# Optimization experiments

Measured on AMD Instinct MI355X. Metric: run time of the kernel, lower is better.

Reference implementation:

```python
import jax, jax.numpy as jnp
import numpy as np

EPS = 1e-5
B, T, C, E, K, D, BN = 8, 2048, 3, 256, 15, 5, 32  # batch, time, channels, embed, kernel, n dilated blocks, bottleneck


def _conv1d(x, w, b, dilation=1):
    # x: [B, Cin, T], w: [Cout, Cin, K] -> [B, Cout, T] ('same' padding)
    k = w.shape[-1]
    pad = dilation * (k - 1) // 2
    y = jax.lax.conv_general_dilated(x, w, (1,), [(pad, pad)], rhs_dilation=(dilation,),
                                     dimension_numbers=('NCH', 'OIH', 'NCH'))
    return y + b[None, :, None]


def _dilated_net(x, w_in, b_in, w_mid, b_mid, w_out, b_out):
    # in->bottleneck conv (dil 1), D dilated convs with doubling dilation, 1x1 out conv
    h = jax.nn.relu(_conv1d(x, w_in, b_in, 1))
    for i in range(w_mid.shape[0]):  # fixed small D, structurally distinct dilations
        h = jax.nn.relu(_conv1d(h, w_mid[i], b_mid[i], 2 ** (i + 1)))
    return _conv1d(h, w_out, b_out, 1)


def setup_inputs() -> dict:
    key = jax.random.key(0)
    ks = jax.random.split(key, 16)
    def w(k, shape, fan_in):
        return jax.random.normal(k, shape, jnp.float32) * (fan_in ** -0.5)
    inp = {
        'query_in': jax.random.normal(ks[0], (B, T, C), jnp.float32),
        'key_in': jax.random.normal(ks[1], (B, T, C), jnp.float32),
    }
    i = 2
    for p in ('q', 'k', 'v'):
        inp[p + '_w_in'] = w(ks[i], (BN, C, K), C * K); i += 1
        inp[p + '_b_in'] = jnp.zeros((BN,), jnp.float32)
        inp[p + '_w_mid'] = w(ks[i], (D, BN, BN, K), BN * K); i += 1
        inp[p + '_b_mid'] = jnp.zeros((D, BN), jnp.float32)
        inp[p + '_w_out'] = w(ks[i], (E, BN, 1), BN); i += 1
        inp[p + '_b_out'] = jnp.zeros((E,), jnp.float32)
    inp['out_w'] = w(ks[i], (C, E), E); i += 1
    inp['out_b'] = jnp.zeros((C,), jnp.float32)
    inp['revin_w'] = jnp.ones((C,), jnp.float32)
    inp['revin_b'] = jnp.zeros((C,), jnp.float32)
    return inp


def reference(query_in, key_in,
              q_w_in, q_b_in, q_w_mid, q_b_mid, q_w_out, q_b_out,
              k_w_in, k_b_in, k_w_mid, k_b_mid, k_w_out, k_b_out,
              v_w_in, v_b_in, v_w_mid, v_b_mid, v_w_out, v_b_out,
              out_w, out_b, revin_w, revin_b):
    # RevIN 'norm': instance stats over time from key_in; query reuses them (recalc_stats=False)
    mean = jnp.mean(key_in, axis=1, keepdims=True)                       # [B,1,C]
    std = jnp.sqrt(jnp.var(key_in, axis=1, keepdims=True) + EPS)         # [B,1,C]
    kn = (((key_in - mean) / std) * revin_w + revin_b).transpose(0, 2, 1)    # [B,C,T]
    qn = (((query_in - mean) / std) * revin_w + revin_b).transpose(0, 2, 1)  # [B,C,T]

    q = _dilated_net(qn, q_w_in, q_b_in, q_w_mid, q_b_mid, q_w_out, q_b_out).transpose(0, 2, 1)  # [B,T,E]
    k = _dilated_net(kn, k_w_in, k_b_in, k_w_mid, k_b_mid, k_w_out, k_b_out).transpose(0, 2, 1)
    v = _dilated_net(kn, v_w_in, v_b_in, v_w_mid, v_b_mid, v_w_out, v_b_out).transpose(0, 2, 1)

    # single-head attention; in_proj is identity (module hardcodes stacked eye), eval -> no dropout
    scale = q.shape[-1] ** -0.5
    attn = jax.nn.softmax(jnp.einsum('bqe,bke->bqk', q * scale, k), axis=-1)  # [B,T,T]
    out = jnp.einsum('bqk,bke->bqe', attn, v)                                  # [B,T,E]
    rec = out @ out_w.T + out_b                                                # [B,T,C]

    # RevIN 'denorm'
    rec = ((rec - revin_b) / revin_w) * std + mean
    return rec
```

## Files before the change

kernel.cpp:

```cpp
#include <hip/hip_runtime.h>
#include <hip/hip_bf16.h>
#include <stdint.h>

#define DEVI __device__ __forceinline__

namespace {

constexpr int B = 8, T = 2048, C = 3, E = 256, KW = 15, BN = 32;
constexpr float EPS = 1e-5f;

constexpr int XPAD = 8;
constexpr int XS   = T + 2*XPAD;
constexpr int HPAD = 224;
constexpr int HS   = T + 2*HPAD;

constexpr size_t O_MEAN = 0;
constexpr size_t O_STD  = 32;
constexpr size_t O_QN   = 64;
constexpr size_t XBUF   = (size_t)B*C*XS;
constexpr size_t O_KN   = O_QN + XBUF;
constexpr size_t HBUF   = (size_t)3*B*BN*HS;
constexpr size_t O_HA   = O_KN + XBUF;
constexpr size_t O_HB   = O_HA + HBUF;
constexpr size_t O_Q    = O_HB + HBUF;
constexpr size_t QBUF_H = (size_t)B*T*E/2;
constexpr size_t O_K    = O_Q + QBUF_H;
constexpr size_t O_V    = O_K + QBUF_H;
constexpr size_t O_PO_HI= O_V + QBUF_H;
constexpr size_t O_WPM  = O_PO_HI;
constexpr size_t O_WPO  = O_WPM + (size_t)245760;
constexpr size_t O_PO_LO= O_QN;
constexpr size_t O_MLM  = O_PO_LO + QBUF_H;
constexpr size_t O_MLL  = O_MLM + (size_t)4*B*T;

typedef __attribute__((ext_vector_type(8))) short bfrag;
typedef __attribute__((ext_vector_type(4))) float f32x4;
typedef __attribute__((ext_vector_type(16))) float f32x16;
typedef __attribute__((ext_vector_type(4))) unsigned int u32x4;
typedef __attribute__((ext_vector_type(2))) unsigned int u32x2;

DEVI short f2bf(float f){
  uint32_t u = __builtin_bit_cast(uint32_t, f);
  u = u + 0x7fffu + ((u >> 16) & 1u);
  return (short)(u >> 16);
}
DEVI float bf2f(unsigned short u){
  uint32_t x = (uint32_t)u << 16;
  return __builtin_bit_cast(float, x);
}
DEVI uint32_t cvtpk(float a, float b){
  uint32_t d;
  asm("v_cvt_pk_bf16_f32 %0, %1, %2" : "=v"(d) : "v"(a), "v"(b));
  return d;
}
DEVI f32x16 vzero16(){
  f32x16 v;
  #pragma unroll
  for (int i = 0; i < 16; i++) v[i] = 0.f;
  return v;
}

DEVI void gload16(const unsigned short* g, short* l){
  __builtin_amdgcn_global_load_lds((const __attribute__((address_space(1))) void*)g,
                                   (__attribute__((address_space(3))) void*)l, 16, 0, 0);
}

__global__ __launch_bounds__(256) void k_prep(
    float* __restrict__ ws,
    const float* __restrict__ query_in, const float* __restrict__ key_in,
    const float* __restrict__ revin_w, const float* __restrict__ revin_b,
    const float* __restrict__ qm, const float* __restrict__ km, const float* __restrict__ vm,
    const float* __restrict__ qo, const float* __restrict__ ko, const float* __restrict__ vo){
  __shared__ float r1[256], r2[256];
  __shared__ float sm, sinv;
  const int r = blockIdx.x;
  if (r < 1536){
    float* row = ws + (r < 768 ? O_HA : O_HB) + (size_t)(r & 767)*HS;
    const int t = threadIdx.x;
    if (t < HPAD) row[t] = 0.f;
    else if (t < 2*HPAD) row[T + t] = 0.f;
  } else if (r == 1536){
    for (int z = threadIdx.x; z < 768; z += 256){
      int buf = z >= 384; int zz = z & 383;
      int rw = zz >> 4; int p = zz & 15;
      float* base = ws + (buf ? O_KN : O_QN) + (size_t)rw*XS;
      base[p < 8 ? p : (XPAD + T + p - 8)] = 0.f;
    }
  } else if (r < 2437){
    unsigned short* wA = (unsigned short*)(ws + O_WPM);
    int p = (r - 1537)*256 + threadIdx.x;
    int j  = p & 7;
    int l  = (p >> 3) & 63;
    int kb = (p >> 9) % 30;
    int netlyr = p / 15360;
    int net = netlyr / 5, lyr = netlyr % 5;
    int o  = l & 31, hi = l >> 5;
    int i  = (kb & 1)*16 + hi*8 + j;
    int kk = kb >> 1;
    const float* src = (net==0 ? qm : (net==1 ? km : vm));
    float w = src[(((size_t)lyr*32 + o)*32 + i)*15 + kk];
    unsigned short wh = (unsigned short)f2bf(w);
    unsigned short wl = (unsigned short)f2bf(w - bf2f(wh));
    size_t base = ((size_t)(netlyr*30 + kb))*1024 + l*8 + j;
    wA[base]       = wh;
    wA[base + 512] = wl;
  } else if (r < 2533){
    float* wpo = ws + O_WPO;
    int idx = (r - 2437)*256 + threadIdx.x;
    int e = idx & 255;
    int i = (idx >> 8) & 31;
    int net = idx >> 13;
    const float* src = (net==0 ? qo : (net==1 ? ko : vo));
    wpo[idx] = src[(size_t)e*32 + i];
  } else {
    const int bc = r - 2533;
    const int b = bc / C, c = bc % C;
    float* meanp = ws + O_MEAN; float* stdp = ws + O_STD;
    float* qn = ws + O_QN;      float* kn = ws + O_KN;
    float s = 0.f, s2 = 0.f;
    for (int t = threadIdx.x; t < T; t += 256){
      float v = key_in[((size_t)(b*T) + t)*C + c];
      s += v; s2 += v*v;
    }
    r1[threadIdx.x] = s; r2[threadIdx.x] = s2;
    __syncthreads();
    for (int st = 128; st > 0; st >>= 1){
      if (threadIdx.x < st){ r1[threadIdx.x] += r1[threadIdx.x+st]; r2[threadIdx.x] += r2[threadIdx.x+st]; }
      __syncthreads();
    }
    if (threadIdx.x == 0){
      float m = r1[0] / (float)T;
      float var = r2[0] / (float)T - m*m;
      float sd = sqrtf(var + EPS);
      meanp[bc] = m; stdp[bc] = sd; sm = m; sinv = 1.f/sd;
    }
    __syncthreads();
    const float m = sm, inv = sinv, wvv = revin_w[c], bvv = revin_b[c];
    for (int t = threadIdx.x; t < T; t += 256){
      size_t src = ((size_t)(b*T) + t)*C + c;
      size_t dst = ((size_t)(b*C) + c)*XS + XPAD + t;
      qn[dst] = (query_in[src] - m) * inv * wvv + bvv;
      kn[dst] = (key_in[src]   - m) * inv * wvv + bvv;
    }
  }
}

__global__ __launch_bounds__(256) void k_conv_in(
    const float* __restrict__ qn, const float* __restrict__ kn,
    const float* __restrict__ wq, const float* __restrict__ bq,
    const float* __restrict__ wk, const float* __restrict__ bk,
    const float* __restrict__ wv, const float* __restrict__ bv,
    float* __restrict__ hout){
  __shared__ float xs[C*XS];
  const int net = blockIdx.x / (B*BN);
  const int rem = blockIdx.x % (B*BN);
  const int b = rem / BN, o = rem % BN;
  const float* x    = (net==0 ? qn : kn) + (size_t)b*C*XS;
  const float* w    = (net==0 ? wq : (net==1 ? wk : wv)) + o*C*KW;
  const float* bias = (net==0 ? bq : (net==1 ? bk : bv));
  for (int i = threadIdx.x; i < C*XS; i += 256) xs[i] = x[i];
  __syncthreads();
  const float bo = bias[o];
  float* orow = hout + (((size_t)(net*B + b))*BN + o)*HS + HPAD;
  for (int j = 0; j < 8; j++){
    int t = j*256 + threadIdx.x;
    float acc = bo;
    #pragma unroll
    for (int c = 0; c < C; c++)
      #pragma unroll
      for (int kk = 0; kk < KW; kk++)
        acc += xs[c*XS + XPAD + t + kk - 7] * w[c*KW + kk];
    orow[t] = fmaxf(acc, 0.f);
  }
}

template<int DIL>
__global__ __launch_bounds__(256) void k_conv_mid(
    const float* __restrict__ hin, float* __restrict__ hout,
    const unsigned short* __restrict__ wA,
    const float* __restrict__ bq, const float* __restrict__ bk, const float* __restrict__ bv,
    int layer){
  constexpr int WT  = 128 + 14*DIL;
  constexpr int NRR = (WT + 15)/16;
  __shared__ __align__(16) unsigned short Xh[WT*40];
  __shared__ __align__(16) unsigned short Xl[WT*40];

  const int net = blockIdx.x >> 7;
  const int rem = blockIdx.x & 127;
  const int b  = rem >> 4;
  const int tt = rem & 15;
  const int netb = net*B + b;
  const int tid  = threadIdx.x;
  const int wv   = __builtin_amdgcn_readfirstlane(tid >> 6);
  const int lane = tid & 63;
  const int l5   = lane & 31;
  const int hi   = lane >> 5;

  {
    const int ip = tid >> 4;
    const int tl = tid & 15;
    const int gt0 = HPAD + tt*128 - 7*DIL;
    const float* r0 = hin + ((size_t)(netb*32 + 2*ip))*HS + gt0;
    const float* r1 = r0 + HS;
    unsigned int* xhw = (unsigned int*)Xh;
    unsigned int* xlw = (unsigned int*)Xl;
    #pragma unroll
    for (int rr = 0; rr < NRR; rr++){
      int t = rr*16 + tl;
      if (t < WT){
        float a = r0[t], bb = r1[t];
        uint32_t hp = cvtpk(a, bb);
        float la = a  - bf2f((unsigned short)(hp & 0xffffu));
        float lb = bb - bf2f((unsigned short)(hp >> 16));
        uint32_t lp = cvtpk(la, lb);
        xhw[t*20 + ip] = hp;
        xlw[t*20 + ip] = lp;
      }
    }
  }
  __syncthreads();

  const unsigned short* wAl = wA + (size_t)(net*5 + layer)*30*1024;
  f32x16 a0 = vzero16(), a1 = vzero16(), a2 = vzero16();
  for (int kb = 0; kb < 30; kb++){
    const int kk  = kb >> 1;
    const int i16 = kb & 1;
    bfrag Ah = *(const bfrag*)(wAl + (size_t)kb*1024 + lane*8);
    bfrag Al = *(const bfrag*)(wAl + (size_t)kb*1024 + 512 + lane*8);
    const int row = wv*32 + l5 + kk*DIL;
    bfrag Bh = *(const bfrag*)&Xh[row*40 + (i16*2 + hi)*8];
    bfrag Bl = *(const bfrag*)&Xl[row*40 + (i16*2 + hi)*8];
    a0 = __builtin_amdgcn_mfma_f32_32x32x16_bf16(Ah, Bh, a0, 0, 0, 0);
    a1 = __builtin_amdgcn_mfma_f32_32x32x16_bf16(Ah, Bl, a1, 0, 0, 0);
    a2 = __builtin_amdgcn_mfma_f32_32x32x16_bf16(Al, Bh, a2, 0, 0, 0);
  }

  const float* bias = (net==0 ? bq : (net==1 ? bk : bv)) + layer*BN;
  const int tg = tt*128 + wv*32 + l5;
  float* obase = hout + ((size_t)netb*32)*HS + HPAD + tg;
  #pragma unroll
  for (int g = 0; g < 4; g++){
    float4 bg = *(const float4*)(bias + g*8 + 4*hi);
    #pragma unroll
    for (int q = 0; q < 4; q++){
      int o = g*8 + 4*hi + q;
      float v = a0[g*4+q] + a1[g*4+q] + a2[g*4+q] + ((const float*)&bg)[q];
      obase[(size_t)o*HS] = fmaxf(v, 0.f);
    }
  }
}

__global__ __launch_bounds__(256) void k_conv_out(
    const float* __restrict__ hin, const float* __restrict__ wpo,
    const float* __restrict__ bq, const float* __restrict__ bk, const float* __restrict__ bv,
    unsigned short* __restrict__ qo, unsigned short* __restrict__ ko, unsigned short* __restrict__ vo){
  const int net = blockIdx.x >> 9;
  const int rem = blockIdx.x & 511;
  const int b = rem >> 6;
  const int tt = (rem & 63) >> 2;
  const int eq = rem & 3;
  const int wave = __builtin_amdgcn_readfirstlane(threadIdx.x >> 6);
  const int lane = threadIdx.x & 63;
  const int t0 = tt*128 + lane*2;
  const int e_base = eq*64 + wave*16;
  const float* wb   = wpo + (size_t)net*32*256 + e_base;
  const float* bias = (net==0 ? bq : (net==1 ? bk : bv)) + e_base;
  float acc[16][2];
  #pragma unroll
  for (int j = 0; j < 16; j++){ acc[j][0] = 0.f; acc[j][1] = 0.f; }
  const float* hb = hin + (((size_t)(net*B + b))*BN)*HS + HPAD + t0;
  for (int i = 0; i < BN; i++){
    const float2 xv = *(const float2*)(hb + (size_t)i*HS);
    const float* wi = wb + i*256;
    #pragma unroll
    for (int j = 0; j < 16; j++){
      const float wj = wi[j];
      acc[j][0] += wj*xv.x; acc[j][1] += wj*xv.y;
    }
  }
  if (net != 2){
    const float scale = (net==0) ? 0.0625f : 1.0f;
    unsigned short* outp = (net==0 ? qo : ko);
    #pragma unroll
    for (int z = 0; z < 2; z++){
      bfrag pk[2];
      #pragma unroll
      for (int j = 0; j < 16; j++)
        pk[j>>3][j&7] = f2bf((acc[j][z] + bias[j]) * scale);
      size_t dst = ((size_t)(b*T) + t0 + z)*E + e_base;
      *(bfrag*)&outp[dst]     = pk[0];
      *(bfrag*)&outp[dst + 8] = pk[1];
    }
  } else {
    unsigned int* vt = (unsigned int*)vo;
    #pragma unroll
    for (int j = 0; j < 16; j++){
      unsigned int lo = (unsigned short)f2bf(acc[j][0] + bias[j]);
      unsigned int hi = (unsigned short)f2bf(acc[j][1] + bias[j]);
      size_t idx = (size_t)(e_base + j)*((size_t)B*T) + (size_t)b*T + t0;
      vt[idx >> 1] = lo | (hi << 16);
    }
  }
}

__global__ __launch_bounds__(256, 2) void k_attn(
    const unsigned short* __restrict__ qbuf, const unsigned short* __restrict__ kbuf,
    const unsigned short* __restrict__ vbufT,
    unsigned short* __restrict__ PO_hi, unsigned short* __restrict__ PO_lo,
    float* __restrict__ MLm, float* __restrict__ MLl){
  __shared__ __align__(16) short Ks[2][32*256];
  __shared__ __align__(16) short Vs[2][256*32];

  const int nid  = ((blockIdx.x & 7) << 6) | (blockIdx.x >> 3);
  const int s    = nid & 3;
  const int qt   = (nid >> 2) & 15;
  const int b    = nid >> 6;
  const int tid  = threadIdx.x;
  const int wv   = __builtin_amdgcn_readfirstlane(tid >> 6);
  const int lane = tid & 63;
  const int l5   = lane & 31;
  const int hi   = lane >> 5;
  const int qrow_base = qt*128 + wv*32;

  bfrag b_q[16];
  {
    const unsigned short* qp = qbuf + ((size_t)(b*T) + qrow_base + l5)*E + hi*8;
    #pragma unroll
    for (int st = 0; st < 16; st++)
      b_q[st] = *(const bfrag*)&qp[st*16];
  }

  f32x16 acc[8];
  #pragma unroll
  for (int nt = 0; nt < 8; nt++) acc[nt] = vzero16();
  float m_run = -1e30f, l_run = 0.f;

  const unsigned short* gks[4]; const unsigned short* gvs[4];
  #pragma unroll
  for (int u = 0; u < 4; u++){
    int lin = u*256 + tid;
    int kr = lin >> 5, kg = lin & 31;
    gks[u] = kbuf + ((size_t)(b*T) + kr)*E + ((kg ^ (kr & 7)) << 3);
    int ve = lin >> 2, vg = lin & 3;
    gvs[u] = vbufT + (size_t)ve*((size_t)B*T) + (size_t)b*T + ((vg ^ ((ve >> 1) & 3)) << 3);
  }
  auto stage = [&](int buf, int j0){
    #pragma unroll
    for (int u = 0; u < 4; u++)
      gload16(gks[u] + (size_t)j0*E, &Ks[buf][u*2048 + wv*512]);
    #pragma unroll
    for (int u = 0; u < 4; u++)
      gload16(gvs[u] + j0, &Vs[buf][u*2048 + wv*512]);
  };

  const int x7 = l5 & 7;
  const int vx = (l5 >> 1) & 3;

  const int kend = s*16 + 16;
  stage(0, s*16*32);
  __syncthreads();
  int cur = 0;

  for (int kbk = s*16; kbk < kend; kbk++){
    if (kbk + 1 < kend) stage(cur ^ 1, (kbk+1)*32);

    f32x16 sac = vzero16();
    __builtin_amdgcn_s_setprio(1);
    #pragma unroll
    for (int st = 0; st < 16; st++){
      bfrag ka = *(const bfrag*)&Ks[cur][l5*256 + ((((st << 1) | hi) ^ x7) << 3)];
      sac = __builtin_amdgcn_mfma_f32_32x32x16_bf16(ka, b_q[st], sac, 0, 0, 0);
    }
    __builtin_amdgcn_s_setprio(0);

    float mloc = sac[0];
    #pragma unroll
    for (int r = 1; r < 16; r++) mloc = fmaxf(mloc, sac[r]);
    mloc = fmaxf(mloc, __shfl_xor(mloc, 32));

    if (__ballot(mloc > m_run + 8.f)){
      float mn = fmaxf(m_run, mloc);
      float alpha = __expf(m_run - mn);
      m_run = mn;
      l_run *= alpha;
      #pragma unroll
      for (int nt = 0; nt < 8; nt++)
        #pragma unroll
        for (int r = 0; r < 16; r++) acc[nt][r] *= alpha;
    }
    float p[16]; float ls = 0.f;
    #pragma unroll
    for (int r = 0; r < 16; r++){
      p[r] = __expf(sac[r] - m_run);
      ls += p[r];
    }
    l_run += ls;

    uint32_t pk[8], xk[8];
    #pragma unroll
    for (int r = 0; r < 8; r++)
      pk[r] = cvtpk(p[2*r], p[2*r+1]);
    #pragma unroll
    for (int r = 0; r < 8; r++) xk[r] = __shfl_xor(pk[r], 32);
    u32x4 w0, w1;
    w0[0] = hi ? xk[2] : pk[0];  w0[1] = hi ? xk[3] : pk[1];
    w0[2] = hi ? pk[2] : xk[0];  w0[3] = hi ? pk[3] : xk[1];
    w1[0] = hi ? xk[6] : pk[4];  w1[1] = hi ? xk[7] : pk[5];
    w1[2] = hi ? pk[6] : xk[4];  w1[3] = hi ? pk[7] : xk[5];
    bfrag pf0 = __builtin_bit_cast(bfrag, w0);
    bfrag pf1 = __builtin_bit_cast(bfrag, w1);

    __builtin_amdgcn_s_setprio(1);
    #pragma unroll
    for (int nt = 0; nt < 8; nt++){
      bfrag v0 = *(const bfrag*)&Vs[cur][(nt*32 + l5)*32 + (((0 | hi) ^ vx) << 3)];
      acc[nt] = __builtin_amdgcn_mfma_f32_32x32x16_bf16(v0, pf0, acc[nt], 0, 0, 0);
      bfrag v1 = *(const bfrag*)&Vs[cur][(nt*32 + l5)*32 + (((2 | hi) ^ vx) << 3)];
      acc[nt] = __builtin_amdgcn_mfma_f32_32x32x16_bf16(v1, pf1, acc[nt], 0, 0, 0);
    }
    __builtin_amdgcn_s_setprio(0);

    __syncthreads();
    cur ^= 1;
  }

  l_run += __shfl_xor(l_run, 32);
  const float inv_l = 1.f / l_run;
  const int row = qrow_base + l5;
  unsigned short* PO = (s < 3) ? (PO_hi + (size_t)s*((size_t)B*T*E)) : PO_lo;
  const size_t off = ((size_t)(b*T) + row)*E;
  #pragma unroll
  for (int nt = 0; nt < 8; nt++){
    #pragma unroll
    for (int g = 0; g < 4; g++){
      const int e0 = nt*32 + 8*g + 4*hi;
      u32x2 wpair;
      wpair[0] = cvtpk(acc[nt][g*4+0]*inv_l, acc[nt][g*4+1]*inv_l);
      wpair[1] = cvtpk(acc[nt][g*4+2]*inv_l, acc[nt][g*4+3]*inv_l);
      *(u32x2*)&PO[off + e0] = wpair;
    }
  }
  if (hi == 0){
    const size_t rm = ((size_t)(s*B + b))*T + row;
    MLm[rm] = m_run;
    MLl[rm] = l_run;
  }
}

__global__ __launch_bounds__(256) void k_comb(
    const unsigned short* __restrict__ PO_hi, const unsigned short* __restrict__ PO_lo,
    const float* __restrict__ MLm, const float* __restrict__ MLl,
    const float* __restrict__ out_w, const float* __restrict__ out_b,
    const float* __restrict__ revin_w, const float* __restrict__ revin_b,
    const float* __restrict__ meanp, const float* __restrict__ stdp,
    float* __restrict__ out){
  __shared__ float wsh[3*E];
  for (int i = threadIdx.x; i < 3*E; i += 256) wsh[i] = out_w[i];
  __syncthreads();
  const int b  = blockIdx.x >> 6;
  const int rt = blockIdx.x & 63;
  const int row = rt*32 + (threadIdx.x >> 3);
  const int c8 = threadIdx.x & 7;
  const int e0 = c8*32;
  float ms[4], ls[4], wn[4];
  #pragma unroll
  for (int s2 = 0; s2 < 4; s2++){
    const size_t rm = ((size_t)(s2*B + b))*T + row;
    ms[s2] = MLm[rm]; ls[s2] = MLl[rm];
  }
  float mx = fmaxf(fmaxf(ms[0], ms[1]), fmaxf(ms[2], ms[3]));
  float wsum = 0.f;
  #pragma unroll
  for (int s2 = 0; s2 < 4; s2++){ wn[s2] = __expf(ms[s2]-mx)*ls[s2]; wsum += wn[s2]; }
  float inv = 1.f/wsum;
  #pragma unroll
  for (int s2 = 0; s2 < 4; s2++) wn[s2] *= inv;
  const unsigned short* ps[4];
  #pragma unroll
  for (int s2 = 0; s2 < 4; s2++){
    const unsigned short* base = (s2 < 3) ? (PO_hi + (size_t)s2*((size_t)B*T*E)) : PO_lo;
    ps[s2] = base + ((size_t)(b*T) + row)*E + e0;
  }
  float pr[3] = {0.f, 0.f, 0.f};
  #pragma unroll
  for (int u = 0; u < 4; u++){
    float v[8] = {0,0,0,0,0,0,0,0};
    #pragma unroll
    for (int s2 = 0; s2 < 4; s2++){
      bfrag a = *(const bfrag*)&ps[s2][u*8];
      #pragma unroll
      for (int z = 0; z < 8; z++) v[z] += wn[s2]*bf2f((unsigned short)a[z]);
    }
    #pragma unroll
    for (int z = 0; z < 8; z++){
      int e = e0 + u*8 + z;
      pr[0] += v[z]*wsh[e];
      pr[1] += v[z]*wsh[E + e];
      pr[2] += v[z]*wsh[2*E + e];
    }
  }
  #pragma unroll
  for (int c = 0; c < 3; c++){
    pr[c] += __shfl_xor(pr[c], 1);
    pr[c] += __shfl_xor(pr[c], 2);
    pr[c] += __shfl_xor(pr[c], 4);
  }
  if (c8 == 0){
    #pragma unroll
    for (int c = 0; c < 3; c++){
      float val = pr[c] + out_b[c];
      val = (val - revin_b[c]) / revin_w[c];
      val = val * stdp[b*C + c] + meanp[b*C + c];
      out[((size_t)(b*T) + row)*C + c] = val;
    }
  }
}

}

extern "C" void kernel_launch(void* const* d_in, const int* in_sizes, int n_in,
                              void* d_out, int out_size, void* d_ws, size_t ws_size,
                              hipStream_t stream){
  const float* query_in = (const float*)d_in[0];
  const float* key_in   = (const float*)d_in[1];
  const float* q_w_in   = (const float*)d_in[2];
  const float* q_b_in   = (const float*)d_in[3];
  const float* q_w_mid  = (const float*)d_in[4];
  const float* q_b_mid  = (const float*)d_in[5];
  const float* q_w_out  = (const float*)d_in[6];
  const float* q_b_out  = (const float*)d_in[7];
  const float* k_w_in   = (const float*)d_in[8];
  const float* k_b_in   = (const float*)d_in[9];
  const float* k_w_mid  = (const float*)d_in[10];
  const float* k_b_mid  = (const float*)d_in[11];
  const float* k_w_out  = (const float*)d_in[12];
  const float* k_b_out  = (const float*)d_in[13];
  const float* v_w_in   = (const float*)d_in[14];
  const float* v_b_in   = (const float*)d_in[15];
  const float* v_w_mid  = (const float*)d_in[16];
  const float* v_b_mid  = (const float*)d_in[17];
  const float* v_w_out  = (const float*)d_in[18];
  const float* v_b_out  = (const float*)d_in[19];
  const float* out_w    = (const float*)d_in[20];
  const float* out_b    = (const float*)d_in[21];
  const float* revin_w  = (const float*)d_in[22];
  const float* revin_b  = (const float*)d_in[23];
  float* ws  = (float*)d_ws;
  float* out = (float*)d_out;

  unsigned short* qb = (unsigned short*)(ws + O_Q);
  unsigned short* kb = (unsigned short*)(ws + O_K);
  unsigned short* vb = (unsigned short*)(ws + O_V);
  unsigned short* PO_hi = (unsigned short*)(ws + O_PO_HI);
  unsigned short* PO_lo = (unsigned short*)(ws + O_PO_LO);
  float* MLm = ws + O_MLM;
  float* MLl = ws + O_MLL;
  unsigned short* wA = (unsigned short*)(ws + O_WPM);
  float* wpo = ws + O_WPO;

  hipLaunchKernelGGL(k_prep, dim3(2557), dim3(256), 0, stream,
                     ws, query_in, key_in, revin_w, revin_b,
                     q_w_mid, k_w_mid, v_w_mid, q_w_out, k_w_out, v_w_out);
  hipLaunchKernelGGL(k_conv_in, dim3(3*B*BN), dim3(256), 0, stream,
                     ws+O_QN, ws+O_KN, q_w_in, q_b_in, k_w_in, k_b_in, v_w_in, v_b_in, ws+O_HA);
  float* ha = ws + O_HA;
  float* hb = ws + O_HB;
  hipLaunchKernelGGL(k_conv_mid<2>,  dim3(384), dim3(256), 0, stream, ha, hb,
                     wA, q_b_mid, k_b_mid, v_b_mid, 0);
  hipLaunchKernelGGL(k_conv_mid<4>,  dim3(384), dim3(256), 0, stream, hb, ha,
                     wA, q_b_mid, k_b_mid, v_b_mid, 1);
  hipLaunchKernelGGL(k_conv_mid<8>,  dim3(384), dim3(256), 0, stream, ha, hb,
                     wA, q_b_mid, k_b_mid, v_b_mid, 2);
  hipLaunchKernelGGL(k_conv_mid<16>, dim3(384), dim3(256), 0, stream, hb, ha,
                     wA, q_b_mid, k_b_mid, v_b_mid, 3);
  hipLaunchKernelGGL(k_conv_mid<32>, dim3(384), dim3(256), 0, stream, ha, hb,
                     wA, q_b_mid, k_b_mid, v_b_mid, 4);
  hipLaunchKernelGGL(k_conv_out, dim3(1536), dim3(256), 0, stream,
                     hb, wpo, q_b_out, k_b_out, v_b_out, qb, kb, vb);
  hipLaunchKernelGGL(k_attn, dim3(B*16*4), dim3(256), 0, stream, qb, kb, vb, PO_hi, PO_lo, MLm, MLl);
  hipLaunchKernelGGL(k_comb, dim3(B*T/32), dim3(256), 0, stream,
                     PO_hi, PO_lo, MLm, MLl, out_w, out_b, revin_w, revin_b, ws+O_MEAN, ws+O_STD, out);
}
```

Before: 283.6 us.

## Store intermediate activations as pre-split bf16 hi/lo in time-major swizzled layout

Intermediate conv activations are now stored as pre-split bf16 hi/lo pairs in a time-major layout (64 shorts per time step), replacing fp32 channel-major rows. Each mid conv layer can then load its tile straight into LDS with swizzled global_load_lds, with no per-layer fp32-to-bf16 split. The input conv is retiled per time chunk so one thread computes 16 output channels. The output conv reads the hi/lo pairs and uses the original weight layout, so the weight-transpose prep pass is dropped. The aim is to cut activation traffic and conversion work between layers, at the cost of hi+lo reconstruction in conv_out and strided weight reads there.

```diff
diff --git a/kernel.cpp b/kernel.cpp
--- a/kernel.cpp
+++ b/kernel.cpp
@@ -28,7 +28,6 @@
 constexpr size_t O_V    = O_K + QBUF_H;
 constexpr size_t O_PO_HI= O_V + QBUF_H;
 constexpr size_t O_WPM  = O_PO_HI;
-constexpr size_t O_WPO  = O_WPM + (size_t)245760;
 constexpr size_t O_PO_LO= O_QN;
 constexpr size_t O_MLM  = O_PO_LO + QBUF_H;
 constexpr size_t O_MLL  = O_MLM + (size_t)4*B*T;
@@ -69,16 +68,22 @@
     float* __restrict__ ws,
     const float* __restrict__ query_in, const float* __restrict__ key_in,
     const float* __restrict__ revin_w, const float* __restrict__ revin_b,
-    const float* __restrict__ qm, const float* __restrict__ km, const float* __restrict__ vm,
-    const float* __restrict__ qo, const float* __restrict__ ko, const float* __restrict__ vo){
+    const float* __restrict__ qm, const float* __restrict__ km, const float* __restrict__ vm){
   __shared__ float r1[256], r2[256];
   __shared__ float sm, sinv;
   const int r = blockIdx.x;
   if (r < 1536){
-    float* row = ws + (r < 768 ? O_HA : O_HB) + (size_t)(r & 767)*HS;
-    const int t = threadIdx.x;
-    if (t < HPAD) row[t] = 0.f;
-    else if (t < 2*HPAD) row[T + t] = 0.f;
+    const int buf  = r >= 768;
+    const int zz   = r & 767;
+    const int netb = zz >> 5;
+    const int chunk= zz & 31;
+    uint32_t* p32 = (uint32_t*)((unsigned short*)(ws + (buf ? O_HB : O_HA)) + (size_t)netb*HS*64);
+    for (int d = threadIdx.x; d < 14*32; d += 256){
+      int rm = d >> 5, wd = d & 31;
+      int hr = chunk*14 + rm;
+      int row = (hr < HPAD) ? hr : (HPAD + T + hr - HPAD);
+      p32[(size_t)row*32 + wd] = 0u;
+    }
   } else if (r == 1536){
     for (int z = threadIdx.x; z < 768; z += 256){
       int buf = z >= 384; int zz = z & 383;
@@ -104,16 +109,8 @@
     size_t base = ((size_t)(netlyr*30 + kb))*1024 + l*8 + j;
     wA[base]       = wh;
     wA[base + 512] = wl;
-  } else if (r < 2533){
-    float* wpo = ws + O_WPO;
-    int idx = (r - 2437)*256 + threadIdx.x;
-    int e = idx & 255;
-    int i = (idx >> 8) & 31;
-    int net = idx >> 13;
-    const float* src = (net==0 ? qo : (net==1 ? ko : vo));
-    wpo[idx] = src[(size_t)e*32 + i];
   } else {
-    const int bc = r - 2533;
+    const int bc = r - 2437;
     const int b = bc / C, c = bc % C;
     float* meanp = ws + O_MEAN; float* stdp = ws + O_STD;
     float* qn = ws + O_QN;      float* kn = ws + O_KN;
@@ -150,40 +147,77 @@
     const float* __restrict__ wq, const float* __restrict__ bq,
     const float* __restrict__ wk, const float* __restrict__ bk,
     const float* __restrict__ wv, const float* __restrict__ bv,
-    float* __restrict__ hout){
-  __shared__ float xs[C*XS];
-  const int net = blockIdx.x / (B*BN);
-  const int rem = blockIdx.x % (B*BN);
-  const int b = rem / BN, o = rem % BN;
+    unsigned short* __restrict__ hout){
+  constexpr int XW = 142;
+  __shared__ float xs[C*XW];
+  const int net = blockIdx.x >> 7;
+  const int rem = blockIdx.x & 127;
+  const int b = rem >> 4, tt = rem & 15;
+  const int netb = net*B + b;
   const float* x    = (net==0 ? qn : kn) + (size_t)b*C*XS;
-  const float* w    = (net==0 ? wq : (net==1 ? wk : wv)) + o*C*KW;
+  const float* w    = (net==0 ? wq : (net==1 ? wk : wv));
   const float* bias = (net==0 ? bq : (net==1 ? bk : bv));
-  for (int i = threadIdx.x; i < C*XS; i += 256) xs[i] = x[i];
+  for (int u = threadIdx.x; u < C*XW; u += 256){
+    int c = u / XW, off = u - c*XW;
+    xs[u] = x[(size_t)c*XS + XPAD + tt*128 - 7 + off];
+  }
   __syncthreads();
-  const float bo = bias[o];
-  float* orow = hout + (((size_t)(net*B + b))*BN + o)*HS + HPAD;
-  for (int j = 0; j < 8; j++){
-    int t = j*256 + threadIdx.x;
-    float acc = bo;
-    #pragma unroll
-    for (int c = 0; c < C; c++)
+  const int wvv  = __builtin_amdgcn_readfirstlane(threadIdx.x >> 6);
+  const int lane = threadIdx.x & 63;
+  const int oh   = wvv & 1;
+  const int tl   = (wvv >> 1)*64 + lane;
+  float acc[16];
+  #pragma unroll
+  for (int j = 0; j < 16; j++) acc[j] = bias[oh*16 + j];
+  #pragma unroll
+  for (int c = 0; c < C; c++)
+    #pragma unroll
+    for (int kk = 0; kk < KW; kk++){
+      const float xv = xs[c*XW + tl + kk];
       #pragma unroll
-      for (int kk = 0; kk < KW; kk++)
-        acc += xs[c*XS + XPAD + t + kk - 7] * w[c*KW + kk];
-    orow[t] = fmaxf(acc, 0.f);
+      for (int j = 0; j < 16; j++)
+        acc[j] += w[(oh*16 + j)*C*KW + c*KW + kk] * xv;
+    }
+  unsigned short* orow = hout + (size_t)netb*HS*64 + (size_t)(HPAD + tt*128 + tl)*64;
+  u32x4 hw0, lw0;
+  #pragma unroll
+  for (int q = 0; q < 4; q++){
+    float v0 = fmaxf(acc[q*4+0], 0.f), v1 = fmaxf(acc[q*4+1], 0.f);
+    float v2 = fmaxf(acc[q*4+2], 0.f), v3 = fmaxf(acc[q*4+3], 0.f);
+    uint32_t h0 = cvtpk(v0, v1), h1 = cvtpk(v2, v3);
+    float l0 = v0 - bf2f((unsigned short)(h0 & 0xffffu));
+    float l1 = v1 - bf2f((unsigned short)(h0 >> 16));
+    float l2 = v2 - bf2f((unsigned short)(h1 & 0xffffu));
+    float l3 = v3 - bf2f((unsigned short)(h1 >> 16));
+    if (q < 2){ hw0[q*2] = h0; hw0[q*2+1] = h1; lw0[q*2] = cvtpk(l0,l1); lw0[q*2+1] = cvtpk(l2,l3); }
+    else {
+      if (q == 2){ hw0[0] = hw0[0]; }
+    }
+    if (q == 1){
+      *(u32x4*)&orow[oh*16]      = hw0;
+      *(u32x4*)&orow[32 + oh*16] = lw0;
+    }
+    if (q >= 2){
+      static_assert(true, "");
+      if (q == 2){ hw0[0] = h0; hw0[1] = h1; lw0[0] = cvtpk(l0,l1); lw0[1] = cvtpk(l2,l3); }
+      else { hw0[2] = h0; hw0[3] = h1; lw0[2] = cvtpk(l0,l1); lw0[3] = cvtpk(l2,l3);
+        *(u32x4*)&orow[oh*16 + 8]      = hw0;
+        *(u32x4*)&orow[32 + oh*16 + 8] = lw0;
+      }
+    }
   }
 }
 
 template<int DIL>
 __global__ __launch_bounds__(256) void k_conv_mid(
-    const float* __restrict__ hin, float* __restrict__ hout,
+    const unsigned short* __restrict__ hin, unsigned short* __restrict__ hout,
     const unsigned short* __restrict__ wA,
     const float* __restrict__ bq, const float* __restrict__ bk, const float* __restrict__ bv,
     int layer){
   constexpr int WT  = 128 + 14*DIL;
-  constexpr int NRR = (WT + 15)/16;
-  __shared__ __align__(16) unsigned short Xh[WT*40];
-  __shared__ __align__(16) unsigned short Xl[WT*40];
+  constexpr int NU  = (WT*8 + 255)/256;
+  constexpr int WTP = NU*32;
+  __shared__ __align__(16) unsigned short Xs[WTP*64];
 
   const int net = blockIdx.x >> 7;
   const int rem = blockIdx.x & 127;
@@ -194,29 +228,15 @@
   const int wv   = __builtin_amdgcn_readfirstlane(tid >> 6);
   const int lane = tid & 63;
   const int l5   = lane & 31;
-  const int hi   = lane >> 5;
-
-  {
-    const int ip = tid >> 4;
-    const int tl = tid & 15;
-    const int gt0 = HPAD + tt*128 - 7*DIL;
-    const float* r0 = hin + ((size_t)(netb*32 + 2*ip))*HS + gt0;
-    const float* r1 = r0 + HS;
-    unsigned int* xhw = (unsigned int*)Xh;
-    unsigned int* xlw = (unsigned int*)Xl;
-    #pragma unroll
-    for (int rr = 0; rr < NRR; rr++){
-      int t = rr*16 + tl;
-      if (t < WT){
-        float a = r0[t], bb = r1[t];
-        uint32_t hp = cvtpk(a, bb);
-        float la = a  - bf2f((unsigned short)(hp & 0xffffu));
-        float lb = bb - bf2f((unsigned short)(hp >> 16));
-        uint32_t lp = cvtpk(la, lb);
-        xhw[t*20 + ip] = hp;
-        xlw[t*20 + ip] = lp;
-      }
-    }
+  const int hiq  = lane >> 5;
+
+  const int t0 = HPAD + tt*128 - 7*DIL;
+  const unsigned short* hsrc = hin + (size_t)netb*HS*64 + (size_t)t0*64;
+  #pragma unroll
+  for (int u = 0; u < NU; u++){
+    int lin = u*256 + tid;
+    int rl = lin >> 3, g = lin & 7;
+    gload16(hsrc + (size_t)rl*64 + ((g ^ (rl & 7)) << 3), (short*)&Xs[u*2048 + wv*512]);
   }
   __syncthreads();
 
@@ -228,8 +248,9 @@
     bfrag Ah = *(const bfrag*)(wAl + (size_t)kb*1024 + lane*8);
     bfrag Al = *(const bfrag*)(wAl + (size_t)kb*1024 + 512 + lane*8);
     const int row = wv*32 + l5 + kk*DIL;
-    bfrag Bh = *(const bfrag*)&Xh[row*40 + (i16*2 + hi)*8];
-    bfrag Bl = *(const bfrag*)&Xl[row*40 + (i16*2 + hi)*8];
+    const int gb  = i16*2 + hiq;
+    bfrag Bh = *(const bfrag*)&Xs[row*64 + (((gb    ) ^ (row & 7)) << 3)];
+    bfrag Bl = *(const bfrag*)&Xs[row*64 + (((4 + gb) ^ (row & 7)) << 3)];
     a0 = __builtin_amdgcn_mfma_f32_32x32x16_bf16(Ah, Bh, a0, 0, 0, 0);
     a1 = __builtin_amdgcn_mfma_f32_32x32x16_bf16(Ah, Bl, a1, 0, 0, 0);
     a2 = __builtin_amdgcn_mfma_f32_32x32x16_bf16(Al, Bh, a2, 0, 0, 0);
@@ -237,22 +258,30 @@
 
   const float* bias = (net==0 ? bq : (net==1 ? bk : bv)) + layer*BN;
   const int tg = tt*128 + wv*32 + l5;
-  float* obase = hout + ((size_t)netb*32)*HS + HPAD + tg;
+  unsigned short* orow = hout + (size_t)netb*HS*64 + (size_t)(HPAD + tg)*64;
   #pragma unroll
   for (int g = 0; g < 4; g++){
-    float4 bg = *(const float4*)(bias + g*8 + 4*hi);
-    #pragma unroll
-    for (int q = 0; q < 4; q++){
-      int o = g*8 + 4*hi + q;
-      float v = a0[g*4+q] + a1[g*4+q] + a2[g*4+q] + ((const float*)&bg)[q];
-      obase[(size_t)o*HS] = fmaxf(v, 0.f);
-    }
+    float v0 = fmaxf(a0[g*4+0]+a1[g*4+0]+a2[g*4+0] + bias[g*8+4*hiq+0], 0.f);
+    float v1 = fmaxf(a0[g*4+1]+a1[g*4+1]+a2[g*4+1] + bias[g*8+4*hiq+1], 0.f);
+    float v2 = fmaxf(a0[g*4+2]+a1[g*4+2]+a2[g*4+2] + bias[g*8+4*hiq+2], 0.f);
+    float v3 = fmaxf(a0[g*4+3]+a1[g*4+3]+a2[g*4+3] + bias[g*8+4*hiq+3], 0.f);
+    uint32_t h0 = cvtpk(v0, v1), h1 = cvtpk(v2, v3);
+    float l0 = v0 - bf2f((unsigned short)(h0 & 0xffffu));
+    float l1 = v1 - bf2f((unsigned short)(h0 >> 16));
+    float l2 = v2 - bf2f((unsigned short)(h1 & 0xffffu));
+    float l3 = v3 - bf2f((unsigned short)(h1 >> 16));
+    u32x2 hw; hw[0] = h0; hw[1] = h1;
+    u32x2 lw; lw[0] = cvtpk(l0, l1); lw[1] = cvtpk(l2, l3);
+    *(u32x2*)&orow[g*8 + hiq*4]      = hw;
+    *(u32x2*)&orow[32 + g*8 + hiq*4] = lw;
   }
 }
 
 __global__ __launch_bounds__(256) void k_conv_out(
-    const float* __restrict__ hin, const float* __restrict__ wpo,
-    const float* __restrict__ bq, const float* __restrict__ bk, const float* __restrict__ bv,
+    const unsigned short* __restrict__ hin,
+    const float* __restrict__ wq, const float* __restrict__ bq,
+    const float* __restrict__ wk, const float* __restrict__ bk,
+    const float* __restrict__ wv, const float* __restrict__ bv,
     unsigned short* __restrict__ qo, unsigned short* __restrict__ ko, unsigned short* __restrict__ vo){
   const int net = blockIdx.x >> 9;
   const int rem = blockIdx.x & 511;
@@ -263,19 +292,27 @@
   const int lane = threadIdx.x & 63;
   const int t0 = tt*128 + lane*2;
   const int e_base = eq*64 + wave*16;
-  const float* wb   = wpo + (size_t)net*32*256 + e_base;
+  const float* w    = (net==0 ? wq : (net==1 ? wk : wv));
   const float* bias = (net==0 ? bq : (net==1 ? bk : bv)) + e_base;
   float acc[16][2];
   #pragma unroll
   for (int j = 0; j < 16; j++){ acc[j][0] = 0.f; acc[j][1] = 0.f; }
-  const float* hb = hin + (((size_t)(net*B + b))*BN)*HS + HPAD + t0;
-  for (int i = 0; i < BN; i++){
-    const float2 xv = *(const float2*)(hb + (size_t)i*HS);
-    const float* wi = wb + i*256;
-    #pragma unroll
-    for (int j = 0; j < 16; j++){
-      const float wj = wi[j];
-      acc[j][0] += wj*xv.x; acc[j][1] += wj*xv.y;
+  const unsigned short* r0 = hin + (size_t)(net*B + b)*HS*64 + (size_t)(HPAD + t0)*64;
+  #pragma unroll
+  for (int g = 0; g < 4; g++){
+    bfrag h0 = *(const bfrag*)&r0[g*8];
+    bfrag l0 = *(const bfrag*)&r0[32 + g*8];
+    bfrag h1 = *(const bfrag*)&r0[64 + g*8];
+    bfrag l1 = *(const bfrag*)&r0[96 + g*8];
+    #pragma unroll
+    for (int ii = 0; ii < 8; ii++){
+      float x0 = bf2f((unsigned short)h0[ii]) + bf2f((unsigned short)l0[ii]);
+      float x1 = bf2f((unsigned short)h1[ii]) + bf2f((unsigned short)l1[ii]);
+      #pragma unroll
+      for (int j = 0; j < 16; j++){
+        const float wj = w[(size_t)(e_base + j)*BN + g*8 + ii];
+        acc[j][0] += wj*x0; acc[j][1] += wj*x1;
+      }
     }
   }
   if (net != 2){
@@ -556,15 +593,14 @@
   float* MLm = ws + O_MLM;
   float* MLl = ws + O_MLL;
   unsigned short* wA = (unsigned short*)(ws + O_WPM);
-  float* wpo = ws + O_WPO;
-
-  hipLaunchKernelGGL(k_prep, dim3(2557), dim3(256), 0, stream,
+  unsigned short* ha = (unsigned short*)(ws + O_HA);
+  unsigned short* hb = (unsigned short*)(ws + O_HB);
+
+  hipLaunchKernelGGL(k_prep, dim3(2461), dim3(256), 0, stream,
                      ws, query_in, key_in, revin_w, revin_b,
-                     q_w_mid, k_w_mid, v_w_mid, q_w_out, k_w_out, v_w_out);
-  hipLaunchKernelGGL(k_conv_in, dim3(3*B*BN), dim3(256), 0, stream,
-                     ws+O_QN, ws+O_KN, q_w_in, q_b_in, k_w_in, k_b_in, v_w_in, v_b_in, ws+O_HA);
-  float* ha = ws + O_HA;
-  float* hb = ws + O_HB;
+                     q_w_mid, k_w_mid, v_w_mid);
+  hipLaunchKernelGGL(k_conv_in, dim3(384), dim3(256), 0, stream,
+                     ws+O_QN, ws+O_KN, q_w_in, q_b_in, k_w_in, k_b_in, v_w_in, v_b_in, ha);
   hipLaunchKernelGGL(k_conv_mid<2>,  dim3(384), dim3(256), 0, stream, ha, hb,
                      wA, q_b_mid, k_b_mid, v_b_mid, 0);
   hipLaunchKernelGGL(k_conv_mid<4>,  dim3(384), dim3(256), 0, stream, hb, ha,
@@ -576,7 +612,7 @@
   hipLaunchKernelGGL(k_conv_mid<32>, dim3(384), dim3(256), 0, stream, ha, hb,
                      wA, q_b_mid, k_b_mid, v_b_mid, 4);
   hipLaunchKernelGGL(k_conv_out, dim3(1536), dim3(256), 0, stream,
-                     hb, wpo, q_b_out, k_b_out, v_b_out, qb, kb, vb);
+                     hb, q_w_out, q_b_out, k_w_out, k_b_out, v_w_out, v_b_out, qb, kb, vb);
   hipLaunchKernelGGL(k_attn, dim3(B*16*4), dim3(256), 0, stream, qb, kb, vb, PO_hi, PO_lo, MLm, MLl);
   hipLaunchKernelGGL(k_comb, dim3(B*T/32), dim3(256), 0, stream,
                      PO_hi, PO_lo, MLm, MLl, out_w, out_b, revin_w, revin_b, ws+O_MEAN, ws+O_STD, out);
```

New measurement: 299.6 us. 5.6% more time.
